# Kernel optimization log

Hardware: AMD Instinct MI355X
Metric: run time of the kernel (lower is better)

Reference implementation:

```python
import jax, jax.numpy as jnp
import numpy as np
from jax import lax

N_C = 1024  # number of FPS centroids (hard-coded in forward)
K = 32      # knn neighbors (hard-coded in forward)


def _fps(x, far0):
    # Faithful to the source: dist is recomputed against ONLY the latest
    # centroid each iteration (the mask/min-update in the source is dead code),
    # then far = argmax(dist).
    B = x.shape[0]
    bidx = jnp.arange(B)

    def step(far, _):
        c = x[bidx, far]                              # [B, C]
        d = jnp.sum((x - c[:, None, :]) ** 2, -1)     # [B, N]
        return jnp.argmax(d, -1), c

    _, cents = lax.scan(step, far0, None, length=N_C)  # cents: [n_c, B, C]
    return jnp.transpose(cents, (1, 0, 2))             # [B, n_c, C]


def _knn_group(x, cent):
    # squared euclidean distances (same argsort order as torch.cdist)
    d2 = (jnp.sum(cent ** 2, -1)[..., None]
          + jnp.sum(x ** 2, -1)[:, None, :]
          - 2.0 * jnp.einsum('bmc,bnc->bmn', cent, x))   # [B, n_c, N]
    _, idx = lax.top_k(-d2, K)                            # [B, n_c, K] smallest dists
    neighbors = jax.vmap(lambda xb, ib: xb[ib])(x, idx)   # [B, n_c, K, C]
    return neighbors


def _conv1x1(h, w, b):
    # 1x1 Conv1d == channel matmul; h: [B, Cin, L], w: [Cout, Cin]
    return jax.nn.relu(jnp.einsum('oi,bil->bol', w, h) + b[None, :, None])


def setup_inputs() -> dict:
    key = jax.random.key(0)
    ks = jax.random.split(key, 20)
    B, N, C = 4, 16384, 3
    num_classes = 3
    p = lambda k, shp: (jax.random.normal(k, shp, jnp.float32) * 0.02)
    return {
        'x': jax.random.normal(ks[0], (B, N, C), jnp.float32),
        'far_init': jax.random.randint(ks[1], (B,), 0, N, jnp.int32),
        'w1': p(ks[2], (64, 3)),    'b1': p(ks[3], (64,)),
        'w2': p(ks[4], (64, 64)),   'b2': p(ks[5], (64,)),
        'w3': p(ks[6], (64, 64)),   'b3': p(ks[7], (64,)),
        'w4': p(ks[8], (128, 64)),  'b4': p(ks[9], (128,)),
        'w5': p(ks[10], (1024, 128)), 'b5': p(ks[11], (1024,)),
        'fw1': p(ks[12], (512, 1024)), 'fb1': p(ks[13], (512,)),
        'fw2': p(ks[14], (256, 512)),  'fb2': p(ks[15], (256,)),
        'fw3': p(ks[16], (num_classes, 256)), 'fb3': p(ks[17], (num_classes,)),
    }


def reference(x, far_init, w1, b1, w2, b2, w3, b3, w4, b4, w5, b5,
              fw1, fb1, fw2, fb2, fw3, fb3):
    B, N, C = x.shape
    cent = _fps(x, far_init)                 # [B, n_c, C]
    neighbors = _knn_group(x, cent)          # [B, n_c, K, C]
    h = jnp.transpose(neighbors, (0, 3, 1, 2)).reshape(B, C, N_C * K)
    h = _conv1x1(h, w1, b1)
    h = _conv1x1(h, w2, b2)
    h = _conv1x1(h, w3, b3)
    h = _conv1x1(h, w4, b4)
    h = _conv1x1(h, w5, b5)                  # [B, 1024, n_c*K]
    g = jnp.max(h, axis=2)                   # global max pool -> [B, 1024]
    g = jax.nn.relu(g @ fw1.T + fb1)
    g = jax.nn.relu(g @ fw2.T + fb2)
    return g @ fw3.T + fb3                   # [B, num_classes]
```

## Files before the change

### kernel.cpp

```cpp
#include <hip/hip_runtime.h>

#define BN  4
#define NPT 16384
#define NCC 1024
#define KNN 32

#define HBINS    2048
#define CCH      2
#define CAND_CAP 768

#define OFF_CCOUNT 0
#define OFF_SCOUNT 64
#define OFF_SBITS  128
#define OFF_POOL   (128 + BN*(NPT/32)*4)
#define OFF_CLIST  (OFF_POOL + BN*NCC*4)
#define OFF_SLIST  (OFF_CLIST + BN*NCC*4)

typedef short bf16x8 __attribute__((ext_vector_type(8)));
typedef float f32x4  __attribute__((ext_vector_type(4)));
typedef float f32x2  __attribute__((ext_vector_type(2)));

__device__ __forceinline__ short f2bf(float f) {
    unsigned u = __float_as_uint(f);
    return (short)((u + 0x7fffu + ((u >> 16) & 1u)) >> 16);
}
__device__ __forceinline__ bf16x8 cvt8(const float* __restrict__ p) {
    bf16x8 v;
#pragma unroll
    for (int j = 0; j < 8; ++j) v[j] = f2bf(p[j]);
    return v;
}

__global__ __launch_bounds__(1024) void fps_kernel(const float* __restrict__ x,
    const int* __restrict__ far_init, int* __restrict__ clist, int* __restrict__ ccount,
    int* __restrict__ scount, unsigned* __restrict__ sbits, float* __restrict__ pool)
{
#pragma clang fp contract(off)
    const int b = blockIdx.x, t = threadIdx.x;
    __shared__ __align__(16) unsigned char seen[NPT];
    __shared__ unsigned long long slot[3];

    if (t < 512) sbits[b*(NPT/32) + t] = 0u;
    pool[b*NCC + t] = 0.0f;
    if (t == 0) { ccount[b] = 0; scount[b] = 0; }

    const float* xb = x + (size_t)b * NPT * 3;
    f32x2 px[8], py[8], pz[8];
#pragma unroll
    for (int r = 0; r < 8; ++r) {
        int ia = t + ((2*r) << 10), ib = ia + 1024;
        px[r] = f32x2{xb[ia*3+0], xb[ib*3+0]};
        py[r] = f32x2{xb[ia*3+1], xb[ib*3+1]};
        pz[r] = f32x2{xb[ia*3+2], xb[ib*3+2]};
    }
    ((uint4*)seen)[t] = make_uint4(0,0,0,0);
    if (t == 0) { slot[0] = 0ull; slot[1] = 0ull; slot[2] = 0ull; }
    int prev_bx = far_init[b];
    __syncthreads();
    int pbs = __builtin_amdgcn_readfirstlane(prev_bx);
    float cx = xb[pbs*3], cy = xb[pbs*3+1], cz = xb[pbs*3+2];

    int done = 0;
    for (int it = 0; it < NCC-1; ++it) {
        const int p = it % 3;
        const f32x2 cX = {cx, cx}, cY = {cy, cy}, cZ = {cz, cz};
        float best = -1.0f; int bi = 0;
#pragma unroll
        for (int r = 0; r < 8; ++r) {
            f32x2 dx = px[r] - cX;
            f32x2 dy = py[r] - cY;
            f32x2 dz = pz[r] - cZ;
            f32x2 m1 = dx * dx;
            f32x2 m2 = dy * dy;
            f32x2 m3 = dz * dz;
            f32x2 s  = (m1 + m2) + m3;
            int ia = t + ((2*r) << 10);
            if (s.x > best) { best = s.x; bi = ia; }
            if (s.y > best) { best = s.y; bi = ia + 1024; }
        }
#pragma unroll
        for (int m = 1; m < 64; m <<= 1) {
            float od = __shfl_xor(best, m, 64);
            int   oi = __shfl_xor(bi,   m, 64);
            if (od > best || (od == best && oi < bi)) { best = od; bi = oi; }
        }
        if ((t & 63) == 0) {
            unsigned long long pk =
                (((unsigned long long)__float_as_uint(best)) << 32)
                | (unsigned)(NPT - 1 - bi);
            atomicMax(&slot[p], pk);
        }
        if (t == 0) seen[prev_bx] = 1;
        __syncthreads();
        int bx = NPT - 1 - (int)(unsigned)(slot[p] & 0xFFFFFFFFull);
        if (t == 0) slot[(it + 2) % 3] = 0ull;
        if (seen[bx]) { done = 1; break; }
        prev_bx = bx;
        int bxs = __builtin_amdgcn_readfirstlane(bx);
        cx = xb[bxs*3]; cy = xb[bxs*3+1]; cz = xb[bxs*3+2];
    }
    if (!done && t == 0) seen[prev_bx] = 1;
    __syncthreads();
#pragma unroll
    for (int j = 0; j < 16; ++j) {
        int idx = t + (j << 10);
        if (seen[idx]) {
            int pos = atomicAdd(&ccount[b], 1);
            clist[b * NCC + pos] = idx;
        }
    }
}

__device__ __forceinline__ unsigned key_of(float px, float py, float pz, float xn,
                                           float cx, float cy, float cz, float cn)
{
    float dot = __fadd_rn(__fadd_rn(__fmul_rn(cx,px), __fmul_rn(cy,py)), __fmul_rn(cz,pz));
    float d2  = __fsub_rn(__fadd_rn(cn, xn), __fmul_rn(2.0f, dot));
    unsigned u = __float_as_uint(d2);
    return u ^ ((u >> 31) ? 0xFFFFFFFFu : 0x80000000u);
}

__device__ __forceinline__ void wave_scan_bins(const unsigned* __restrict__ H,
    int nbins, int rem, int lane, int* __restrict__ out_bin, int* __restrict__ out_below)
{
    int per = nbins >> 6;
    int base = lane * per;
    unsigned part = 0;
    for (int q = 0; q < per; ++q) part += H[base + q];
    unsigned inc = part;
#pragma unroll
    for (int m = 1; m < 64; m <<= 1) {
        unsigned u = __shfl_up(inc, m, 64);
        if (lane >= m) inc += u;
    }
    unsigned exc = inc - part;
    unsigned long long mk = __ballot(exc < (unsigned)rem && inc >= (unsigned)rem);
    int src = __ffsll((long long)mk) - 1;
    if (lane == src) {
        unsigned run = exc; int bb = base;
        for (int q = 0; q < per; ++q) {
            unsigned h = H[base + q];
            if (run + h >= (unsigned)rem) { bb = base + q; break; }
            run += h;
        }
        *out_bin = bb; *out_below = (int)run;
    }
}

__global__ __launch_bounds__(1024) void knn_kernel(const float* __restrict__ x,
    const int* __restrict__ clist, const int* __restrict__ ccount,
    unsigned* __restrict__ sbits, int* __restrict__ slist, int* __restrict__ scount)
{
    const int b = blockIdx.y, t = threadIdx.x;
    const int lane = t & 63, w = t >> 6;
    const int cnt = ccount[b];
    const int cbase = blockIdx.x * CCH;
    if (cbase >= cnt) return;
    const float* xb = x + (size_t)b * NPT * 3;

    __shared__ unsigned hist[CCH * HBINS];
    __shared__ unsigned cand[CCH * CAND_CAP];
    __shared__ float cpx[CCH], cpy[CCH], cpz[CCH], cpn[CCH];
    __shared__ unsigned candCnt[CCH];
    __shared__ int s_bb[CCH], s_below[CCH], s_rrem[CCH], s_need[CCH], s_pref[CCH];
    __shared__ unsigned s_tau[CCH];
    __shared__ int s_tbin, s_tbelow;

    if (t < CCH) {
        int ci = clist[b * NCC + min(cbase + t, cnt - 1)];
        float cx = xb[ci*3], cy = xb[ci*3+1], cz = xb[ci*3+2];
        cpx[t] = cx; cpy[t] = cy; cpz[t] = cz;
        cpn[t] = __fadd_rn(__fadd_rn(__fmul_rn(cx,cx), __fmul_rn(cy,cy)), __fmul_rn(cz,cz));
        candCnt[t] = 0;
    }
    for (int i = t; i < CCH * HBINS; i += 1024) hist[i] = 0;
    __syncthreads();

    unsigned keys[NPT/1024][CCH];
#pragma unroll
    for (int j = 0; j < NPT/1024; ++j) {
        int i = t + (j << 10);
        float px = xb[i*3], py = xb[i*3+1], pz = xb[i*3+2];
        float xn = __fadd_rn(__fadd_rn(__fmul_rn(px,px), __fmul_rn(py,py)), __fmul_rn(pz,pz));
#pragma unroll
        for (int c = 0; c < CCH; ++c) {
            unsigned key = key_of(px,py,pz,xn, cpx[c],cpy[c],cpz[c],cpn[c]);
            keys[j][c] = key;
            atomicAdd(&hist[c*HBINS + (key >> 21)], 1u);
        }
    }
    __syncthreads();

    if (w < CCH)
        wave_scan_bins(&hist[w*HBINS], HBINS, KNN, lane, &s_bb[w], &s_below[w]);
    __syncthreads();
    if (t < CCH) s_rrem[t] = KNN - s_below[t];
    __syncthreads();

#pragma unroll
    for (int j = 0; j < NPT/1024; ++j) {
#pragma unroll
        for (int c = 0; c < CCH; ++c) {
            unsigned key = keys[j][c];
            if ((int)(key >> 21) == s_bb[c]) {
                unsigned pos = atomicAdd(&candCnt[c], 1u);
                if (pos < CAND_CAP) cand[c*CAND_CAP + pos] = key;
            }
        }
    }
    __syncthreads();

    if (w < CCH) {
        unsigned cc = candCnt[w];
        if (cc <= CAND_CAP) {
            int r = s_rrem[w] - 1;
            const unsigned* C = &cand[w*CAND_CAP];
            for (int idx = lane; idx < (int)cc; idx += 64) {
                unsigned k = C[idx]; int rank = 0;
                for (int q = 0; q < (int)cc; ++q) {
                    unsigned kq = C[q];
                    rank += (kq < k || (kq == k && q < idx)) ? 1 : 0;
                }
                if (rank == r) s_tau[w] = k;
            }
            if (lane == 0) s_need[w] = 0;
        } else if (lane == 0) s_need[w] = 1;
    }
    __syncthreads();

    for (int c = 0; c < CCH; ++c) {
        if (s_need[c]) {
            const float cx = cpx[c], cy = cpy[c], cz = cpz[c], cn = cpn[c];
            for (int i = t; i < HBINS; i += 1024) hist[i] = 0;
            __syncthreads();
            for (int j = 0; j < NPT/1024; ++j) {
                int i = t + (j << 10);
                float px = xb[i*3], py = xb[i*3+1], pz = xb[i*3+2];
                float xn = __fadd_rn(__fadd_rn(__fmul_rn(px,px), __fmul_rn(py,py)), __fmul_rn(pz,pz));
                unsigned key = key_of(px,py,pz,xn, cx,cy,cz,cn);
                if ((int)(key >> 21) == s_bb[c]) atomicAdd(&hist[(key >> 10) & 2047u], 1u);
            }
            __syncthreads();
            if (w == 0) wave_scan_bins(hist, HBINS, s_rrem[c], lane, &s_tbin, &s_tbelow);
            __syncthreads();
            if (t == 0) { s_pref[c] = (s_bb[c] << 11) | s_tbin; s_rrem[c] -= s_tbelow; }
            __syncthreads();
            for (int i = t; i < 1024; i += 1024) hist[i] = 0;
            __syncthreads();
            for (int j = 0; j < NPT/1024; ++j) {
                int i = t + (j << 10);
                float px = xb[i*3], py = xb[i*3+1], pz = xb[i*3+2];
                float xn = __fadd_rn(__fadd_rn(__fmul_rn(px,px), __fmul_rn(py,py)), __fmul_rn(pz,pz));
                unsigned key = key_of(px,py,pz,xn, cx,cy,cz,cn);
                if ((int)(key >> 10) == s_pref[c]) atomicAdd(&hist[key & 1023u], 1u);
            }
            __syncthreads();
            if (w == 0) wave_scan_bins(hist, 1024, s_rrem[c], lane, &s_tbin, &s_tbelow);
            __syncthreads();
            if (t == 0) s_tau[c] = (((unsigned)s_pref[c]) << 10) | (unsigned)s_tbin;
            __syncthreads();
        }
    }
    __syncthreads();

#pragma unroll
    for (int j = 0; j < NPT/1024; ++j) {
        int i = t + (j << 10);
        bool sel = false;
#pragma unroll
        for (int c = 0; c < CCH; ++c) sel |= (keys[j][c] <= s_tau[c]);
        if (sel) {
            unsigned bit = 1u << (i & 31);
            unsigned old = atomicOr(&sbits[b*(NPT/32) + (i >> 5)], bit);
            if (!(old & bit)) {
                int pos = atomicAdd(&scount[b], 1);
                slist[b * NPT + pos] = i;
            }
        }
    }
}

#define MFMA16(a, bfr, c) __builtin_amdgcn_mfma_f32_16x16x32_bf16(a, bfr, c, 0, 0, 0)

__global__ __launch_bounds__(1024) void mlp_kernel(const float* __restrict__ x,
    const int* __restrict__ sel_list, const int* __restrict__ sel_count,
    const float* __restrict__ w1, const float* __restrict__ b1,
    const float* __restrict__ w2, const float* __restrict__ b2,
    const float* __restrict__ w3, const float* __restrict__ b3,
    const float* __restrict__ w4, const float* __restrict__ b4,
    const float* __restrict__ w5, const float* __restrict__ b5,
    float* __restrict__ pool)
{
    const int b = blockIdx.y, z = blockIdx.z, t = threadIdx.x;
    const int cnt = sel_count[b];
    if ((blockIdx.x << 6) >= cnt) return;
    const int lane = t & 63;
    const int w    = __builtin_amdgcn_readfirstlane(t >> 6);
    const int m    = lane & 15, quad = lane >> 4;

    __shared__ __align__(16) short A1[64 * 72];
    __shared__ __align__(16) short A2[64 * 72];
    __shared__ __align__(16) short A3[64 * 136];
    __shared__ float sx[3 * 64];

    const int ocA = (w >> 2) * 16 + m;
    bf16x8 bw2[2], bw3[2], bw4[2][2], bw5[4];
#pragma unroll
    for (int ks = 0; ks < 2; ++ks) {
        bw2[ks] = cvt8(w2 + ocA*64 + ks*32 + quad*8);
        bw3[ks] = cvt8(w3 + ocA*64 + ks*32 + quad*8);
    }
    int oc4i[2];
#pragma unroll
    for (int r2 = 0; r2 < 2; ++r2) {
        oc4i[r2] = ((w >> 2) + 4*r2) * 16 + m;
#pragma unroll
        for (int ks = 0; ks < 2; ++ks)
            bw4[r2][ks] = cvt8(w4 + oc4i[r2]*64 + ks*32 + quad*8);
    }
    const int oc5 = z*256 + w*16 + m;
#pragma unroll
    for (int ks = 0; ks < 4; ++ks)
        bw5[ks] = cvt8(w5 + oc5*128 + ks*32 + quad*8);
    const float bias2 = b2[ocA], bias3 = b3[ocA];
    const float bias4_0 = b4[oc4i[0]], bias4_1 = b4[oc4i[1]];
    const float bias5 = b5[oc5];
    float w1v[4][3], b1v[4];
#pragma unroll
    for (int i = 0; i < 4; ++i) {
        int oc = w*4 + i;
        w1v[i][0] = w1[oc*3+0]; w1v[i][1] = w1[oc*3+1]; w1v[i][2] = w1[oc*3+2];
        b1v[i] = b1[oc];
    }
    const int pt0 = (w & 3) * 16;

    for (int base = blockIdx.x << 6; base < cnt; base += (32 << 6)) {
        const int npts = min(64, cnt - base);
        __syncthreads();
        if (t < 64) {
            int idx = sel_list[b * NPT + base + min(t, npts - 1)];
            const float* xp = x + ((size_t)b * NPT + idx) * 3;
            sx[t] = xp[0]; sx[64 + t] = xp[1]; sx[128 + t] = xp[2];
        }
        __syncthreads();
        {
            float x0 = sx[lane], x1 = sx[64 + lane], x2 = sx[128 + lane];
#pragma unroll
            for (int i = 0; i < 4; ++i) {
                float acc = fmaf(x2, w1v[i][2], fmaf(x1, w1v[i][1],
                             fmaf(x0, w1v[i][0], b1v[i])));
                A1[lane*72 + w*4 + i] = f2bf(fmaxf(acc, 0.0f));
            }
        }
        __syncthreads();
        {
            bf16x8 a0 = *(const bf16x8*)&A1[(pt0 + m)*72 + quad*8];
            bf16x8 a1 = *(const bf16x8*)&A1[(pt0 + m)*72 + 32 + quad*8];
            f32x4 d = {0.f, 0.f, 0.f, 0.f};
            d = MFMA16(a0, bw2[0], d);
            d = MFMA16(a1, bw2[1], d);
#pragma unroll
            for (int r = 0; r < 4; ++r)
                A2[(pt0 + quad*4 + r)*72 + ocA] = f2bf(fmaxf(d[r] + bias2, 0.0f));
        }
        __syncthreads();
        {
            bf16x8 a0 = *(const bf16x8*)&A2[(pt0 + m)*72 + quad*8];
            bf16x8 a1 = *(const bf16x8*)&A2[(pt0 + m)*72 + 32 + quad*8];
            f32x4 d = {0.f, 0.f, 0.f, 0.f};
            d = MFMA16(a0, bw3[0], d);
            d = MFMA16(a1, bw3[1], d);
#pragma unroll
            for (int r = 0; r < 4; ++r)
                A1[(pt0 + quad*4 + r)*72 + ocA] = f2bf(fmaxf(d[r] + bias3, 0.0f));
        }
        __syncthreads();
        {
            bf16x8 a0 = *(const bf16x8*)&A1[(pt0 + m)*72 + quad*8];
            bf16x8 a1 = *(const bf16x8*)&A1[(pt0 + m)*72 + 32 + quad*8];
#pragma unroll
            for (int r2 = 0; r2 < 2; ++r2) {
                f32x4 d = {0.f, 0.f, 0.f, 0.f};
                d = MFMA16(a0, bw4[r2][0], d);
                d = MFMA16(a1, bw4[r2][1], d);
                float bs = r2 ? bias4_1 : bias4_0;
#pragma unroll
                for (int r = 0; r < 4; ++r)
                    A3[(pt0 + quad*4 + r)*136 + oc4i[r2]] = f2bf(fmaxf(d[r] + bs, 0.0f));
            }
        }
        __syncthreads();
        {
            float vm = 0.0f;
#pragma unroll
            for (int pt4 = 0; pt4 < 4; ++pt4) {
                const int q0 = pt4 * 16;
                f32x4 d = {0.f, 0.f, 0.f, 0.f};
#pragma unroll
                for (int ks = 0; ks < 4; ++ks) {
                    bf16x8 a = *(const bf16x8*)&A3[(q0 + m)*136 + ks*32 + quad*8];
                    d = MFMA16(a, bw5[ks], d);
                }
#pragma unroll
                for (int r = 0; r < 4; ++r)
                    vm = fmaxf(vm, fmaxf(d[r] + bias5, 0.0f));
            }
            vm = fmaxf(vm, __shfl_xor(vm, 16, 64));
            vm = fmaxf(vm, __shfl_xor(vm, 32, 64));
            if (lane < 16)
                atomicMax((int*)&pool[b*NCC + z*256 + w*16 + lane], __float_as_int(vm));
        }
    }
}

__global__ __launch_bounds__(1024) void head_kernel(const float* __restrict__ pool,
    const float* __restrict__ fw1, const float* __restrict__ fb1,
    const float* __restrict__ fw2, const float* __restrict__ fb2,
    const float* __restrict__ fw3, const float* __restrict__ fb3,
    float* __restrict__ out)
{
    const int b = blockIdx.x, t = threadIdx.x;
    const int lane = t & 63;
    const int w = __builtin_amdgcn_readfirstlane(t >> 6);
    __shared__ float g[1024], h1[512], h2[256];
    g[t] = pool[b*NCC + t];
    __syncthreads();
#pragma unroll
    for (int i = 0; i < 32; ++i) {
        int o = w * 32 + i;
        float acc = 0.0f;
#pragma unroll
        for (int j = 0; j < 16; ++j) {
            int k = lane + (j << 6);
            acc += g[k] * fw1[o*1024 + k];
        }
#pragma unroll
        for (int m = 1; m < 64; m <<= 1) acc += __shfl_xor(acc, m, 64);
        if (lane == 0) h1[o] = fmaxf(acc + fb1[o], 0.0f);
    }
    __syncthreads();
#pragma unroll
    for (int i = 0; i < 16; ++i) {
        int o = w * 16 + i;
        float acc = 0.0f;
#pragma unroll
        for (int j = 0; j < 8; ++j) {
            int k = lane + (j << 6);
            acc += h1[k] * fw2[o*512 + k];
        }
#pragma unroll
        for (int m = 1; m < 64; m <<= 1) acc += __shfl_xor(acc, m, 64);
        if (lane == 0) h2[o] = fmaxf(acc + fb2[o], 0.0f);
    }
    __syncthreads();
    if (w < 3) {
        float acc = 0.0f;
#pragma unroll
        for (int j = 0; j < 4; ++j) {
            int k = lane + (j << 6);
            acc += h2[k] * fw3[w*256 + k];
        }
#pragma unroll
        for (int m = 1; m < 64; m <<= 1) acc += __shfl_xor(acc, m, 64);
        if (lane == 0) out[b*3 + w] = acc + fb3[w];
    }
}

extern "C" void kernel_launch(void* const* d_in, const int* in_sizes, int n_in,
                              void* d_out, int out_size, void* d_ws, size_t ws_size,
                              hipStream_t stream)
{
    const float* x    = (const float*)d_in[0];
    const int*   far0 = (const int*)  d_in[1];
    const float *w1 = (const float*)d_in[2],  *b1 = (const float*)d_in[3];
    const float *w2 = (const float*)d_in[4],  *b2 = (const float*)d_in[5];
    const float *w3 = (const float*)d_in[6],  *b3 = (const float*)d_in[7];
    const float *w4 = (const float*)d_in[8],  *b4 = (const float*)d_in[9];
    const float *w5 = (const float*)d_in[10], *b5 = (const float*)d_in[11];
    const float *fw1 = (const float*)d_in[12], *fb1 = (const float*)d_in[13];
    const float *fw2 = (const float*)d_in[14], *fb2 = (const float*)d_in[15];
    const float *fw3 = (const float*)d_in[16], *fb3 = (const float*)d_in[17];

    char* ws = (char*)d_ws;
    int*      ccount = (int*)     (ws + OFF_CCOUNT);
    int*      scount = (int*)     (ws + OFF_SCOUNT);
    unsigned* sbits  = (unsigned*)(ws + OFF_SBITS);
    float*    pool   = (float*)   (ws + OFF_POOL);
    int*      clist  = (int*)     (ws + OFF_CLIST);
    int*      slist  = (int*)     (ws + OFF_SLIST);

    fps_kernel<<<BN, 1024, 0, stream>>>(x, far0, clist, ccount, scount, sbits, pool);
    knn_kernel<<<dim3(NCC/CCH, BN), 1024, 0, stream>>>(x, clist, ccount, sbits, slist, scount);
    mlp_kernel<<<dim3(32, BN, 4), 1024, 0, stream>>>(x, slist, scount,
        w1,b1, w2,b2, w3,b3, w4,b4, w5,b5, pool);
    head_kernel<<<BN, 1024, 0, stream>>>(pool, fw1,fb1, fw2,fb2, fw3,fb3, (float*)d_out);
}
```

Before: 184.9 us.

## Split classifier head into three kernels spread across many blocks

The single-block-per-batch head kernel is replaced by three kernels: FC1 runs on 16x4 blocks, FC2 on 8x4 blocks, and FC3 on 4 small blocks. Intermediate activations go through global workspace buffers. This spreads the 2MB fw1 weight read over many CUs instead of four, in exchange for two extra kernel launches and global round trips.

```diff
diff --git a/kernel.cpp b/kernel.cpp
--- a/kernel.cpp
+++ b/kernel.cpp
@@ -14,7 +14,9 @@
 #define OFF_SBITS  128
 #define OFF_POOL   (128 + BN*(NPT/32)*4)
 #define OFF_CLIST  (OFF_POOL + BN*NCC*4)
-#define OFF_SLIST  (OFF_CLIST + BN*NCC*4)
+#define OFF_H1     (OFF_CLIST + BN*NCC*4)
+#define OFF_H2     (OFF_H1 + BN*512*4)
+#define OFF_SLIST  (OFF_H2 + BN*256*4)
 
 typedef short bf16x8 __attribute__((ext_vector_type(8)));
 typedef float f32x4  __attribute__((ext_vector_type(4)));
@@ -413,21 +415,18 @@
     }
 }
 
-__global__ __launch_bounds__(1024) void head_kernel(const float* __restrict__ pool,
+__global__ __launch_bounds__(1024) void head1_kernel(const float* __restrict__ pool,
     const float* __restrict__ fw1, const float* __restrict__ fb1,
-    const float* __restrict__ fw2, const float* __restrict__ fb2,
-    const float* __restrict__ fw3, const float* __restrict__ fb3,
-    float* __restrict__ out)
-{
-    const int b = blockIdx.x, t = threadIdx.x;
-    const int lane = t & 63;
-    const int w = __builtin_amdgcn_readfirstlane(t >> 6);
-    __shared__ float g[1024], h1[512], h2[256];
+    float* __restrict__ h1g)
+{
+    const int bo = blockIdx.x, b = blockIdx.y, t = threadIdx.x;
+    const int lane = t & 63, w = t >> 6;
+    __shared__ float g[1024];
     g[t] = pool[b*NCC + t];
     __syncthreads();
 #pragma unroll
-    for (int i = 0; i < 32; ++i) {
-        int o = w * 32 + i;
+    for (int i = 0; i < 2; ++i) {
+        int o = bo * 32 + w * 2 + i;
         float acc = 0.0f;
 #pragma unroll
         for (int j = 0; j < 16; ++j) {
@@ -436,12 +435,22 @@
         }
 #pragma unroll
         for (int m = 1; m < 64; m <<= 1) acc += __shfl_xor(acc, m, 64);
-        if (lane == 0) h1[o] = fmaxf(acc + fb1[o], 0.0f);
-    }
-    __syncthreads();
-#pragma unroll
-    for (int i = 0; i < 16; ++i) {
-        int o = w * 16 + i;
+        if (lane == 0) h1g[b*512 + o] = fmaxf(acc + fb1[o], 0.0f);
+    }
+}
+
+__global__ __launch_bounds__(1024) void head2_kernel(const float* __restrict__ h1g,
+    const float* __restrict__ fw2, const float* __restrict__ fb2,
+    float* __restrict__ h2g)
+{
+    const int bo = blockIdx.x, b = blockIdx.y, t = threadIdx.x;
+    const int lane = t & 63, w = t >> 6;
+    __shared__ float h1[512];
+    if (t < 512) h1[t] = h1g[b*512 + t];
+    __syncthreads();
+#pragma unroll
+    for (int i = 0; i < 2; ++i) {
+        int o = bo * 32 + w * 2 + i;
         float acc = 0.0f;
 #pragma unroll
         for (int j = 0; j < 8; ++j) {
@@ -450,8 +459,18 @@
         }
 #pragma unroll
         for (int m = 1; m < 64; m <<= 1) acc += __shfl_xor(acc, m, 64);
-        if (lane == 0) h2[o] = fmaxf(acc + fb2[o], 0.0f);
-    }
+        if (lane == 0) h2g[b*256 + o] = fmaxf(acc + fb2[o], 0.0f);
+    }
+}
+
+__global__ __launch_bounds__(256) void head3_kernel(const float* __restrict__ h2g,
+    const float* __restrict__ fw3, const float* __restrict__ fb3,
+    float* __restrict__ out)
+{
+    const int b = blockIdx.x, t = threadIdx.x;
+    const int lane = t & 63, w = t >> 6;
+    __shared__ float h2[256];
+    h2[t] = h2g[b*256 + t];
     __syncthreads();
     if (w < 3) {
         float acc = 0.0f;
@@ -487,11 +506,15 @@
     unsigned* sbits  = (unsigned*)(ws + OFF_SBITS);
     float*    pool   = (float*)   (ws + OFF_POOL);
     int*      clist  = (int*)     (ws + OFF_CLIST);
+    float*    h1g    = (float*)   (ws + OFF_H1);
+    float*    h2g    = (float*)   (ws + OFF_H2);
     int*      slist  = (int*)     (ws + OFF_SLIST);
 
     fps_kernel<<<BN, 1024, 0, stream>>>(x, far0, clist, ccount, scount, sbits, pool);
     knn_kernel<<<dim3(NCC/CCH, BN), 1024, 0, stream>>>(x, clist, ccount, sbits, slist, scount);
     mlp_kernel<<<dim3(32, BN, 4), 1024, 0, stream>>>(x, slist, scount,
         w1,b1, w2,b2, w3,b3, w4,b4, w5,b5, pool);
-    head_kernel<<<BN, 1024, 0, stream>>>(pool, fw1,fb1, fw2,fb2, fw3,fb3, (float*)d_out);
-}
+    head1_kernel<<<dim3(16, BN), 1024, 0, stream>>>(pool, fw1, fb1, h1g);
+    head2_kernel<<<dim3(8, BN), 1024, 0, stream>>>(h1g, fw2, fb2, h2g);
+    head3_kernel<<<BN, 256, 0, stream>>>(h2g, fw3, fb3, (float*)d_out);
+}
```

Result: faster. 160.0 us (-13.5%).
